# Kernel optimization log

Measured on AMD Instinct MI355X. Metric: run time of the kernel, lower is better.

## Reference

```python
import jax, jax.numpy as jnp
import numpy as np

B, T, C, H = 8, 2048, 256, 4
D = C // H  # head_dim = 64
SCALE = D ** -0.5


def setup_inputs() -> dict:
    key = jax.random.key(0)
    ks = jax.random.split(key, 5)
    return {
        "x": jax.random.normal(ks[0], (B, T, C), dtype=jnp.float32),
        "Wqkv": jax.random.normal(ks[1], (C, 3 * C), dtype=jnp.float32) * (C ** -0.5),
        "bqkv": jax.random.normal(ks[2], (3 * C,), dtype=jnp.float32) * 0.02,
        "Wproj": jax.random.normal(ks[3], (C, C), dtype=jnp.float32) * (C ** -0.5),
        "bproj": jax.random.normal(ks[4], (C,), dtype=jnp.float32) * 0.02,
    }


def reference(x, Wqkv, bqkv, Wproj, bproj):
    b, t, c = x.shape
    # QKV projection -> (3, B, H, T, D) matching torch permute(2,0,3,1,4)
    qkv = (x @ Wqkv + bqkv).reshape(b, t, 3, H, D)
    qkv = jnp.transpose(qkv, (2, 0, 3, 1, 4))
    q, k, v = qkv[0], qkv[1], qkv[2]  # each (B, H, T, D)
    # Full T x T scores (faithful to the original non-fused implementation)
    attn = jnp.einsum("bhqd,bhkd->bhqk", q, k) * SCALE
    causal = jnp.triu(jnp.ones((t, t), dtype=bool), k=1)  # True above diagonal
    attn = jnp.where(causal, -jnp.inf, attn)
    attn = jax.nn.softmax(attn, axis=-1)
    # dropout is identity in eval mode
    out = jnp.einsum("bhqk,bhkd->bhqd", attn, v)  # (B, H, T, D)
    out = jnp.transpose(out, (0, 2, 1, 3)).reshape(b, t, c)
    return out @ Wproj + bproj
```

## Files before the change

kernel.cpp:

```cpp
#include <hip/hip_runtime.h>
#include <hip/hip_bf16.h>
#include <math.h>

#define BATCH 8
#define SEQ   2048
#define CH    256
#define NH    4
#define HD    64
#define NQB   (SEQ / 64)
#define QSCALE 0.18033688011112042f

typedef short  bfrag __attribute__((ext_vector_type(8)));
typedef float  ffrag __attribute__((ext_vector_type(4)));
typedef unsigned short ushort_t;

__device__ __forceinline__ unsigned short f2bf(float f) {
    union { float f; unsigned int u; } v; v.f = f;
    unsigned int r = v.u + 0x7FFF + ((v.u >> 16) & 1);
    return (unsigned short)(r >> 16);
}
__device__ __forceinline__ unsigned int pack2(float a, float b) {
    const __hip_bfloat162 p = __float22bfloat162_rn(make_float2(a, b));
    return *(const unsigned int*)&p;
}

#define WQN (CH * 3 * CH)
#define WPN (CH * CH)
#define XN  (BATCH * SEQ * CH)
#define XN8 (XN / 8)

__global__ __launch_bounds__(256) void prep_kernel(
    const float* __restrict__ x,
    const float* __restrict__ Wqkv, const float* __restrict__ Wproj,
    ushort_t* __restrict__ xb,
    ushort_t* __restrict__ WqkvT, ushort_t* __restrict__ WprojT) {
    const int fid = blockIdx.x * 256 + threadIdx.x;
    if (fid < XN8) {
        const float4 a = *(const float4*)&x[(size_t)fid * 8];
        const float4 c = *(const float4*)&x[(size_t)fid * 8 + 4];
        uint4 pk;
        pk.x = pack2(a.x, a.y); pk.y = pack2(a.z, a.w);
        pk.z = pack2(c.x, c.y); pk.w = pack2(c.z, c.w);
        *(uint4*)&xb[(size_t)fid * 8] = pk;
    } else {
        const int id = fid - XN8;
        if (id < WQN) {
            const int n = id >> 8, k = id & 255;
            WqkvT[n * CH + k] = f2bf(Wqkv[k * (3 * CH) + n]);
        } else if (id < WQN + WPN) {
            const int i = id - WQN;
            const int n = i >> 8, k = i & 255;
            WprojT[n * CH + k] = f2bf(Wproj[k * CH + n]);
        }
    }
}

#define GLS 72

__global__ __launch_bounds__(256) void qkv_mfma_kernel(
    const ushort_t* __restrict__ xb, const ushort_t* __restrict__ Wt,
    const float* __restrict__ bias,
    ushort_t* __restrict__ Qb, ushort_t* __restrict__ Kb,
    ushort_t* __restrict__ Vtb) {
    __shared__ ushort_t smem[2 * 128 * GLS];
    ushort_t* As = smem;
    ushort_t* Bs = smem + 128 * GLS;

    const int tid = threadIdx.x;
    const int wv  = tid >> 6;
    const int ln  = tid & 63;
    const int l15 = ln & 15;
    const int l4  = ln >> 4;
    const int wr  = wv >> 1;
    const int wc  = wv & 1;
    const int n0  = blockIdx.x * 128;
    const int m0  = blockIdx.y * 128;

    ffrag acc[4][4];
    #pragma unroll
    for (int i = 0; i < 4; i++)
        #pragma unroll
        for (int j = 0; j < 4; j++) acc[i][j] = (ffrag){0.f, 0.f, 0.f, 0.f};

    for (int k0 = 0; k0 < CH; k0 += 64) {
        #pragma unroll
        for (int r = 0; r < 4; r++) {
            const int fid = tid + r * 256;
            const int row = fid >> 3, c8 = (fid & 7) * 8;
            *(uint4*)&As[row * GLS + c8] = *(const uint4*)&xb[(size_t)(m0 + row) * CH + k0 + c8];
            *(uint4*)&Bs[row * GLS + c8] = *(const uint4*)&Wt[(n0 + row) * CH + k0 + c8];
        }
        __syncthreads();
        #pragma unroll
        for (int kk = 0; kk < 64; kk += 32) {
            bfrag a[4], b[4];
            #pragma unroll
            for (int i = 0; i < 4; i++)
                a[i] = *(const bfrag*)&As[(wr * 64 + i * 16 + l15) * GLS + kk + l4 * 8];
            #pragma unroll
            for (int j = 0; j < 4; j++)
                b[j] = *(const bfrag*)&Bs[(wc * 64 + j * 16 + l15) * GLS + kk + l4 * 8];
            #pragma unroll
            for (int i = 0; i < 4; i++)
                #pragma unroll
                for (int j = 0; j < 4; j++)
                    acc[i][j] = __builtin_amdgcn_mfma_f32_16x16x32_bf16(a[i], b[j], acc[i][j], 0, 0, 0);
        }
        __syncthreads();
    }

    const int mat = n0 >> 8;
    const int b   = m0 >> 11;
    const int t0  = m0 & (SEQ - 1);
    ushort_t (*T)[136] = (ushort_t(*)[136])smem;

    if (mat < 2) {
        const float sc = (mat == 0) ? QSCALE : 1.0f;
        #pragma unroll
        for (int j = 0; j < 4; j++) {
            const int n_local = wc * 64 + j * 16 + l15;
            const float bj = bias[n0 + n_local];
            #pragma unroll
            for (int i = 0; i < 4; i++) {
                const int m_base = wr * 64 + i * 16 + l4 * 4;
                #pragma unroll
                for (int r = 0; r < 4; r++)
                    T[m_base + r][n_local] = f2bf((acc[i][j][r] + bj) * sc);
            }
        }
        __syncthreads();
        ushort_t* dst = (mat == 0) ? Qb : Kb;
        #pragma unroll
        for (int rr = 0; rr < 8; rr++) {
            const int fid = tid + rr * 256;
            const int row = fid >> 4;
            const int c8  = (fid & 15) * 8;
            const int n_glob = n0 + c8;
            const int h = (n_glob >> 6) & 3;
            const int d = n_glob & 63;
            *(uint4*)&dst[((size_t)((b * NH + h) * SEQ) + t0 + row) * HD + d] =
                *(const uint4*)&T[row][c8];
        }
    } else {
        #pragma unroll
        for (int j = 0; j < 4; j++) {
            const int n_local = wc * 64 + j * 16 + l15;
            const float bj = bias[n0 + n_local];
            #pragma unroll
            for (int i = 0; i < 4; i++) {
                const int m_base = wr * 64 + i * 16 + l4 * 4;
                ushort4 pk;
                pk.x = f2bf(acc[i][j][0] + bj);
                pk.y = f2bf(acc[i][j][1] + bj);
                pk.z = f2bf(acc[i][j][2] + bj);
                pk.w = f2bf(acc[i][j][3] + bj);
                *(ushort4*)&T[n_local][m_base] = pk;
            }
        }
        __syncthreads();
        #pragma unroll
        for (int rr = 0; rr < 8; rr++) {
            const int fid = tid + rr * 256;
            const int row = fid >> 4;
            const int c8  = (fid & 15) * 8;
            const int n_glob = n0 + row;
            const int h = (n_glob >> 6) & 3;
            const int d = n_glob & 63;
            *(uint4*)&Vtb[(size_t)((b * NH + h) * HD + d) * SEQ + t0 + c8] =
                *(const uint4*)&T[row][c8];
        }
    }
}

__global__ __launch_bounds__(256, 4) void attn_mfma_kernel(
    const ushort_t* __restrict__ Qb, const ushort_t* __restrict__ Kb,
    const ushort_t* __restrict__ Vtb, ushort_t* __restrict__ out) {
    __shared__ ushort_t Ps[64 * 64];
    __shared__ ushort_t KV[4 * 64 * 64];

    const int tid = threadIdx.x;
    const int wv  = tid >> 6;
    const int ln  = tid & 63;
    const int l15 = ln & 15;
    const int l4  = ln >> 4;
    const int e   = l15 & 7;

    const int L  = blockIdx.x;
    const int g  = L & 255;
    const int s4 = L >> 8;
    const int v  = g >> 5;
    const int qb = (s4 == 0) ? (31 - v) : (s4 == 1) ? (16 + v) : (s4 == 2) ? (15 - v) : v;
    const int bh = g & 31;
    const int b  = bh >> 2;
    const int h  = bh & 3;

    const ushort_t* Qp = Qb + ((size_t)(bh * SEQ + qb * 64 + wv * 16 + l15)) * HD + l4 * 8;
    const bfrag bq0 = *(const bfrag*)Qp;
    const bfrag bq1 = *(const bfrag*)(Qp + 32);

    const ushort_t* Kbase = Kb  + (size_t)bh * SEQ * HD;
    const ushort_t* Vbase = Vtb + (size_t)bh * HD * SEQ;
    const int srow  = tid >> 3;
    const int sc    = tid & 7;
    const int goffA = srow * 64 + sc * 8;
    const int voffA = srow * SEQ + sc * 8;
    const int soffA = srow * 64 + ((sc ^ (srow & 7)) * 8);

    const int kf0 = l15 * 64 + ((l4 ^ e) * 8);
    const int pf0 = (wv * 16 + l15) * 64 + ((l4 ^ e) * 8);
    const int pp  = e >> 1;
    const int pwb = (wv * 16 + l15) * 64 + (((l4 >> 1) ^ (e & 1)) * 8) + (l4 & 1) * 4;

    uint4 kK0, kK1, kV0, kV1;
    kK0 = *(const uint4*)&Kbase[goffA];
    kK1 = *(const uint4*)&Kbase[goffA + 32 * 64];
    kV0 = *(const uint4*)&Vbase[voffA];
    kV1 = *(const uint4*)&Vbase[voffA + 32 * SEQ];
    *(uint4*)&KV[soffA]          = kK0;
    *(uint4*)&KV[soffA + 2048]   = kK1;
    *(uint4*)&KV[8192 + soffA]        = kV0;
    *(uint4*)&KV[8192 + soffA + 2048] = kV1;
    if (qb >= 1) {
        kK0 = *(const uint4*)&Kbase[4096 + goffA];
        kK1 = *(const uint4*)&Kbase[4096 + goffA + 32 * 64];
        kV0 = *(const uint4*)&Vbase[64 + voffA];
        kV1 = *(const uint4*)&Vbase[64 + voffA + 32 * SEQ];
    }

    ffrag o[4];
    #pragma unroll
    for (int n = 0; n < 4; n++) o[n] = (ffrag){0.f, 0.f, 0.f, 0.f};
    float l_q = 0.f;
    const int qg_l = qb * 64 + wv * 16 + l15;

    for (int kt = 0; kt <= qb; kt++) {
        if (kt > 0) {
            const int kb = (kt & 1) * 4096;
            *(uint4*)&KV[kb + soffA]          = kK0;
            *(uint4*)&KV[kb + soffA + 2048]   = kK1;
            *(uint4*)&KV[8192 + kb + soffA]        = kV0;
            *(uint4*)&KV[8192 + kb + soffA + 2048] = kV1;
            if (kt < qb) {
                const ushort_t* Kp  = Kbase + (kt + 1) * 4096;
                const ushort_t* Vtp = Vbase + (kt + 1) * 64;
                kK0 = *(const uint4*)&Kp[goffA];
                kK1 = *(const uint4*)&Kp[goffA + 32 * 64];
                kV0 = *(const uint4*)&Vtp[voffA];
                kV1 = *(const uint4*)&Vtp[voffA + 32 * SEQ];
            }
        }
        __syncthreads();

        const ushort_t* Kbuf = KV + (kt & 1) * 4096;
        const ushort_t* Vbuf = KV + 8192 + (kt & 1) * 4096;

        ffrag s[4];
        #pragma unroll
        for (int n = 0; n < 4; n++) {
            const bfrag ak0 = *(const bfrag*)&Kbuf[n * 1024 + kf0];
            const bfrag ak1 = *(const bfrag*)&Kbuf[n * 1024 + (kf0 ^ 32)];
            ffrag z = (ffrag){0.f, 0.f, 0.f, 0.f};
            z = __builtin_amdgcn_mfma_f32_16x16x32_bf16(ak0, bq0, z, 0, 0, 0);
            z = __builtin_amdgcn_mfma_f32_16x16x32_bf16(ak1, bq1, z, 0, 0, 0);
            s[n] = z;
        }
        if (kt == qb) {
            #pragma unroll
            for (int n = 0; n < 4; n++)
                #pragma unroll
                for (int r = 0; r < 4; r++)
                    if (kt * 64 + n * 16 + l4 * 4 + r > qg_l) s[n][r] = -INFINITY;
        }

        float rs = 0.f;
        #pragma unroll
        for (int n = 0; n < 4; n++)
            #pragma unroll
            for (int r = 0; r < 4; r++) {
                const float p = __builtin_amdgcn_exp2f(s[n][r]);
                s[n][r] = p;
                rs += p;
            }
        rs += __shfl_xor(rs, 16);
        rs += __shfl_xor(rs, 32);
        l_q += rs;

        #pragma unroll
        for (int n = 0; n < 4; n++) {
            uint2 pk;
            pk.x = pack2(s[n][0], s[n][1]);
            pk.y = pack2(s[n][2], s[n][3]);
            *(uint2*)&Ps[pwb + ((n ^ pp) << 4)] = pk;
        }

        const bfrag ap0 = *(const bfrag*)&Ps[pf0];
        const bfrag ap1 = *(const bfrag*)&Ps[pf0 ^ 32];
        #pragma unroll
        for (int n = 0; n < 4; n++) {
            const bfrag av0 = *(const bfrag*)&Vbuf[n * 1024 + kf0];
            const bfrag av1 = *(const bfrag*)&Vbuf[n * 1024 + (kf0 ^ 32)];
            o[n] = __builtin_amdgcn_mfma_f32_16x16x32_bf16(av0, ap0, o[n], 0, 0, 0);
            o[n] = __builtin_amdgcn_mfma_f32_16x16x32_bf16(av1, ap1, o[n], 0, 0, 0);
        }
    }

    const float li = 1.0f / l_q;
    const int tq = qb * 64 + wv * 16 + l15;
    ushort_t* op = out + (size_t)(b * SEQ + tq) * CH + h * HD;
    #pragma unroll
    for (int n = 0; n < 4; n++) {
        ushort4 pk;
        pk.x = f2bf(o[n][0] * li);
        pk.y = f2bf(o[n][1] * li);
        pk.z = f2bf(o[n][2] * li);
        pk.w = f2bf(o[n][3] * li);
        *(ushort4*)&op[n * 16 + l4 * 4] = pk;
    }
}

__global__ __launch_bounds__(256) void proj_mfma_kernel(
    const ushort_t* __restrict__ Ab, const ushort_t* __restrict__ Wt,
    const float* __restrict__ bias, float* __restrict__ O) {
    __shared__ ushort_t smem[(128 + 64) * GLS];
    ushort_t* As = smem;
    ushort_t* Bs = smem + 128 * GLS;

    const int tid = threadIdx.x;
    const int wv  = tid >> 6;
    const int ln  = tid & 63;
    const int l15 = ln & 15;
    const int l4  = ln >> 4;
    const int wr  = wv >> 1;
    const int wc  = wv & 1;
    const int n0  = blockIdx.x * 64;
    const int m0  = blockIdx.y * 128;

    ffrag acc[4][2];
    #pragma unroll
    for (int i = 0; i < 4; i++)
        #pragma unroll
        for (int j = 0; j < 2; j++) acc[i][j] = (ffrag){0.f, 0.f, 0.f, 0.f};

    for (int k0 = 0; k0 < CH; k0 += 64) {
        #pragma unroll
        for (int r = 0; r < 4; r++) {
            const int fid = tid + r * 256;
            const int row = fid >> 3, c8 = (fid & 7) * 8;
            *(uint4*)&As[row * GLS + c8] = *(const uint4*)&Ab[(size_t)(m0 + row) * CH + k0 + c8];
        }
        #pragma unroll
        for (int r = 0; r < 2; r++) {
            const int fid = tid + r * 256;
            const int row = fid >> 3, c8 = (fid & 7) * 8;
            *(uint4*)&Bs[row * GLS + c8] = *(const uint4*)&Wt[(n0 + row) * CH + k0 + c8];
        }
        __syncthreads();
        #pragma unroll
        for (int kk = 0; kk < 64; kk += 32) {
            bfrag a[4], b[2];
            #pragma unroll
            for (int i = 0; i < 4; i++)
                a[i] = *(const bfrag*)&As[(wr * 64 + i * 16 + l15) * GLS + kk + l4 * 8];
            #pragma unroll
            for (int j = 0; j < 2; j++)
                b[j] = *(const bfrag*)&Bs[(wc * 32 + j * 16 + l15) * GLS + kk + l4 * 8];
            #pragma unroll
            for (int i = 0; i < 4; i++)
                #pragma unroll
                for (int j = 0; j < 2; j++)
                    acc[i][j] = __builtin_amdgcn_mfma_f32_16x16x32_bf16(a[i], b[j], acc[i][j], 0, 0, 0);
        }
        __syncthreads();
    }

    #pragma unroll
    for (int j = 0; j < 2; j++) {
        const int n = n0 + wc * 32 + j * 16 + l15;
        const float bj = bias[n];
        #pragma unroll
        for (int i = 0; i < 4; i++) {
            const int m = m0 + wr * 64 + i * 16 + l4 * 4;
            #pragma unroll
            for (int r = 0; r < 4; r++)
                O[(size_t)(m + r) * CH + n] = acc[i][j][r] + bj;
        }
    }
}

extern "C" void kernel_launch(void* const* d_in, const int* in_sizes, int n_in,
                              void* d_out, int out_size, void* d_ws, size_t ws_size,
                              hipStream_t stream) {
    const float* x     = (const float*)d_in[0];
    const float* Wqkv  = (const float*)d_in[1];
    const float* bqkv  = (const float*)d_in[2];
    const float* Wproj = (const float*)d_in[3];
    const float* bproj = (const float*)d_in[4];
    float* out = (float*)d_out;

    const size_t BHTD = (size_t)BATCH * NH * SEQ * HD;
    ushort_t* WqkvT  = (ushort_t*)d_ws;
    ushort_t* WprojT = WqkvT + (size_t)3 * CH * CH;
    ushort_t* Qb     = WprojT + (size_t)CH * CH;
    ushort_t* Kb     = Qb + BHTD;
    ushort_t* Vtb    = Kb + BHTD;
    ushort_t* attn_b = Vtb + BHTD;
    ushort_t* xb     = attn_b;

    const int M = BATCH * SEQ;

    {
        const int total = XN8 + WQN + WPN;
        prep_kernel<<<(total + 255) / 256, 256, 0, stream>>>(x, Wqkv, Wproj, xb, WqkvT, WprojT);
    }
    {
        dim3 grid((3 * CH) / 128, M / 128);
        qkv_mfma_kernel<<<grid, 256, 0, stream>>>(xb, WqkvT, bqkv, Qb, Kb, Vtb);
    }
    {
        attn_mfma_kernel<<<dim3(NQB * BATCH * NH), 256, 0, stream>>>(Qb, Kb, Vtb, attn_b);
    }
    {
        dim3 grid(CH / 64, M / 128);
        proj_mfma_kernel<<<grid, 256, 0, stream>>>(attn_b, WprojT, bproj, out);
    }
}
```

Baseline: 135.7 us.

## Process 128 query rows per attention block to double K/V tile reuse

Each attention block now covers a 128-row query tile, with each wavefront handling two 16-row subtiles, so every K/V tile staged in shared memory feeds twice as many MFMAs. This halves the global and LDS traffic for K/V per query row and halves the grid to 512 blocks, with a reworked causal pairing of tiles to balance load. The cost is more registers per thread (occupancy hint lowered to 2), a larger P buffer, and fewer blocks to spread over the CUs. Causal masking now covers the last two key tiles of the diagonal.

```diff
diff --git a/kernel.cpp b/kernel.cpp
--- a/kernel.cpp
+++ b/kernel.cpp
@@ -7,7 +7,6 @@
 #define CH    256
 #define NH    4
 #define HD    64
-#define NQB   (SEQ / 64)
 #define QSCALE 0.18033688011112042f
 
 typedef short  bfrag __attribute__((ext_vector_type(8)));
@@ -172,10 +171,10 @@
     }
 }
 
-__global__ __launch_bounds__(256, 4) void attn_mfma_kernel(
+__global__ __launch_bounds__(256, 2) void attn_mfma_kernel(
     const ushort_t* __restrict__ Qb, const ushort_t* __restrict__ Kb,
     const ushort_t* __restrict__ Vtb, ushort_t* __restrict__ out) {
-    __shared__ ushort_t Ps[64 * 64];
+    __shared__ ushort_t Ps[128 * 64];
     __shared__ ushort_t KV[4 * 64 * 64];
 
     const int tid = threadIdx.x;
@@ -187,16 +186,20 @@
 
     const int L  = blockIdx.x;
     const int g  = L & 255;
-    const int s4 = L >> 8;
+    const int s2 = L >> 8;
     const int v  = g >> 5;
-    const int qb = (s4 == 0) ? (31 - v) : (s4 == 1) ? (16 + v) : (s4 == 2) ? (15 - v) : v;
+    const int qt = (s2 == 0) ? (15 - v) : v;
     const int bh = g & 31;
     const int b  = bh >> 2;
     const int h  = bh & 3;
-
-    const ushort_t* Qp = Qb + ((size_t)(bh * SEQ + qb * 64 + wv * 16 + l15)) * HD + l4 * 8;
-    const bfrag bq0 = *(const bfrag*)Qp;
-    const bfrag bq1 = *(const bfrag*)(Qp + 32);
+    const int nkt  = 2 * qt + 2;
+    const int qrow = qt * 128 + wv * 32;
+
+    const ushort_t* Qp0 = Qb + ((size_t)(bh * SEQ + qrow + l15)) * HD + l4 * 8;
+    const bfrag bq00 = *(const bfrag*)Qp0;
+    const bfrag bq01 = *(const bfrag*)(Qp0 + 32);
+    const bfrag bq10 = *(const bfrag*)(Qp0 + 16 * HD);
+    const bfrag bq11 = *(const bfrag*)(Qp0 + 16 * HD + 32);
 
     const ushort_t* Kbase = Kb  + (size_t)bh * SEQ * HD;
     const ushort_t* Vbase = Vtb + (size_t)bh * HD * SEQ;
@@ -206,10 +209,12 @@
     const int voffA = srow * SEQ + sc * 8;
     const int soffA = srow * 64 + ((sc ^ (srow & 7)) * 8);
 
-    const int kf0 = l15 * 64 + ((l4 ^ e) * 8);
-    const int pf0 = (wv * 16 + l15) * 64 + ((l4 ^ e) * 8);
-    const int pp  = e >> 1;
-    const int pwb = (wv * 16 + l15) * 64 + (((l4 >> 1) ^ (e & 1)) * 8) + (l4 & 1) * 4;
+    const int kf0  = l15 * 64 + ((l4 ^ e) * 8);
+    const int pf00 = (wv * 32 + l15) * 64 + ((l4 ^ e) * 8);
+    const int pf10 = pf00 + 16 * 64;
+    const int pp   = e >> 1;
+    const int pwb0 = (wv * 32 + l15) * 64 + (((l4 >> 1) ^ (e & 1)) * 8) + (l4 & 1) * 4;
+    const int pwb1 = pwb0 + 16 * 64;
 
     uint4 kK0, kK1, kV0, kV1;
     kK0 = *(const uint4*)&Kbase[goffA];
@@ -220,27 +225,29 @@
     *(uint4*)&KV[soffA + 2048]   = kK1;
     *(uint4*)&KV[8192 + soffA]        = kV0;
     *(uint4*)&KV[8192 + soffA + 2048] = kV1;
-    if (qb >= 1) {
-        kK0 = *(const uint4*)&Kbase[4096 + goffA];
-        kK1 = *(const uint4*)&Kbase[4096 + goffA + 32 * 64];
-        kV0 = *(const uint4*)&Vbase[64 + voffA];
-        kV1 = *(const uint4*)&Vbase[64 + voffA + 32 * SEQ];
-    }
-
-    ffrag o[4];
+    kK0 = *(const uint4*)&Kbase[4096 + goffA];
+    kK1 = *(const uint4*)&Kbase[4096 + goffA + 32 * 64];
+    kV0 = *(const uint4*)&Vbase[64 + voffA];
+    kV1 = *(const uint4*)&Vbase[64 + voffA + 32 * SEQ];
+
+    ffrag o0[4], o1[4];
     #pragma unroll
-    for (int n = 0; n < 4; n++) o[n] = (ffrag){0.f, 0.f, 0.f, 0.f};
-    float l_q = 0.f;
-    const int qg_l = qb * 64 + wv * 16 + l15;
-
-    for (int kt = 0; kt <= qb; kt++) {
+    for (int n = 0; n < 4; n++) {
+        o0[n] = (ffrag){0.f, 0.f, 0.f, 0.f};
+        o1[n] = (ffrag){0.f, 0.f, 0.f, 0.f};
+    }
+    float l0 = 0.f, l1 = 0.f;
+    const int qg0 = qrow + l15;
+    const int qg1 = qg0 + 16;
+
+    for (int kt = 0; kt < nkt; kt++) {
         if (kt > 0) {
             const int kb = (kt & 1) * 4096;
             *(uint4*)&KV[kb + soffA]          = kK0;
             *(uint4*)&KV[kb + soffA + 2048]   = kK1;
             *(uint4*)&KV[8192 + kb + soffA]        = kV0;
             *(uint4*)&KV[8192 + kb + soffA + 2048] = kV1;
-            if (kt < qb) {
+            if (kt < nkt - 1) {
                 const ushort_t* Kp  = Kbase + (kt + 1) * 4096;
                 const ushort_t* Vtp = Vbase + (kt + 1) * 64;
                 kK0 = *(const uint4*)&Kp[goffA];
@@ -254,67 +261,94 @@
         const ushort_t* Kbuf = KV + (kt & 1) * 4096;
         const ushort_t* Vbuf = KV + 8192 + (kt & 1) * 4096;
 
-        ffrag s[4];
+        ffrag s0[4], s1[4];
         #pragma unroll
         for (int n = 0; n < 4; n++) {
             const bfrag ak0 = *(const bfrag*)&Kbuf[n * 1024 + kf0];
             const bfrag ak1 = *(const bfrag*)&Kbuf[n * 1024 + (kf0 ^ 32)];
-            ffrag z = (ffrag){0.f, 0.f, 0.f, 0.f};
-            z = __builtin_amdgcn_mfma_f32_16x16x32_bf16(ak0, bq0, z, 0, 0, 0);
-            z = __builtin_amdgcn_mfma_f32_16x16x32_bf16(ak1, bq1, z, 0, 0, 0);
-            s[n] = z;
-        }
-        if (kt == qb) {
+            ffrag z0 = (ffrag){0.f, 0.f, 0.f, 0.f};
+            z0 = __builtin_amdgcn_mfma_f32_16x16x32_bf16(ak0, bq00, z0, 0, 0, 0);
+            z0 = __builtin_amdgcn_mfma_f32_16x16x32_bf16(ak1, bq01, z0, 0, 0, 0);
+            s0[n] = z0;
+            ffrag z1 = (ffrag){0.f, 0.f, 0.f, 0.f};
+            z1 = __builtin_amdgcn_mfma_f32_16x16x32_bf16(ak0, bq10, z1, 0, 0, 0);
+            z1 = __builtin_amdgcn_mfma_f32_16x16x32_bf16(ak1, bq11, z1, 0, 0, 0);
+            s1[n] = z1;
+        }
+        if (kt >= nkt - 2) {
             #pragma unroll
             for (int n = 0; n < 4; n++)
                 #pragma unroll
-                for (int r = 0; r < 4; r++)
-                    if (kt * 64 + n * 16 + l4 * 4 + r > qg_l) s[n][r] = -INFINITY;
-        }
-
-        float rs = 0.f;
+                for (int r = 0; r < 4; r++) {
+                    const int kk_ = kt * 64 + n * 16 + l4 * 4 + r;
+                    if (kk_ > qg0) s0[n][r] = -INFINITY;
+                    if (kk_ > qg1) s1[n][r] = -INFINITY;
+                }
+        }
+
+        float rs0 = 0.f, rs1 = 0.f;
         #pragma unroll
         for (int n = 0; n < 4; n++)
             #pragma unroll
             for (int r = 0; r < 4; r++) {
-                const float p = __builtin_amdgcn_exp2f(s[n][r]);
-                s[n][r] = p;
-                rs += p;
+                const float p0 = __builtin_amdgcn_exp2f(s0[n][r]);
+                s0[n][r] = p0;
+                rs0 += p0;
+                const float p1 = __builtin_amdgcn_exp2f(s1[n][r]);
+                s1[n][r] = p1;
+                rs1 += p1;
             }
-        rs += __shfl_xor(rs, 16);
-        rs += __shfl_xor(rs, 32);
-        l_q += rs;
+        rs0 += __shfl_xor(rs0, 16);
+        rs0 += __shfl_xor(rs0, 32);
+        l0 += rs0;
+        rs1 += __shfl_xor(rs1, 16);
+        rs1 += __shfl_xor(rs1, 32);
+        l1 += rs1;
 
         #pragma unroll
         for (int n = 0; n < 4; n++) {
-            uint2 pk;
-            pk.x = pack2(s[n][0], s[n][1]);
-            pk.y = pack2(s[n][2], s[n][3]);
-            *(uint2*)&Ps[pwb + ((n ^ pp) << 4)] = pk;
-        }
-
-        const bfrag ap0 = *(const bfrag*)&Ps[pf0];
-        const bfrag ap1 = *(const bfrag*)&Ps[pf0 ^ 32];
+            uint2 pk0, pk1;
+            pk0.x = pack2(s0[n][0], s0[n][1]);
+            pk0.y = pack2(s0[n][2], s0[n][3]);
+            *(uint2*)&Ps[pwb0 + ((n ^ pp) << 4)] = pk0;
+            pk1.x = pack2(s1[n][0], s1[n][1]);
+            pk1.y = pack2(s1[n][2], s1[n][3]);
+            *(uint2*)&Ps[pwb1 + ((n ^ pp) << 4)] = pk1;
+        }
+
+        const bfrag ap00 = *(const bfrag*)&Ps[pf00];
+        const bfrag ap01 = *(const bfrag*)&Ps[pf00 ^ 32];
+        const bfrag ap10 = *(const bfrag*)&Ps[pf10];
+        const bfrag ap11 = *(const bfrag*)&Ps[pf10 ^ 32];
         #pragma unroll
         for (int n = 0; n < 4; n++) {
             const bfrag av0 = *(const bfrag*)&Vbuf[n * 1024 + kf0];
             const bfrag av1 = *(const bfrag*)&Vbuf[n * 1024 + (kf0 ^ 32)];
-            o[n] = __builtin_amdgcn_mfma_f32_16x16x32_bf16(av0, ap0, o[n], 0, 0, 0);
-            o[n] = __builtin_amdgcn_mfma_f32_16x16x32_bf16(av1, ap1, o[n], 0, 0, 0);
-        }
-    }
-
-    const float li = 1.0f / l_q;
-    const int tq = qb * 64 + wv * 16 + l15;
-    ushort_t* op = out + (size_t)(b * SEQ + tq) * CH + h * HD;
+            o0[n] = __builtin_amdgcn_mfma_f32_16x16x32_bf16(av0, ap00, o0[n], 0, 0, 0);
+            o0[n] = __builtin_amdgcn_mfma_f32_16x16x32_bf16(av1, ap01, o0[n], 0, 0, 0);
+            o1[n] = __builtin_amdgcn_mfma_f32_16x16x32_bf16(av0, ap10, o1[n], 0, 0, 0);
+            o1[n] = __builtin_amdgcn_mfma_f32_16x16x32_bf16(av1, ap11, o1[n], 0, 0, 0);
+        }
+    }
+
+    const float li0 = 1.0f / l0;
+    const float li1 = 1.0f / l1;
+    const int tq0 = qrow + l15;
+    ushort_t* op0 = out + (size_t)(b * SEQ + tq0) * CH + h * HD;
+    ushort_t* op1 = op0 + 16 * CH;
     #pragma unroll
     for (int n = 0; n < 4; n++) {
-        ushort4 pk;
-        pk.x = f2bf(o[n][0] * li);
-        pk.y = f2bf(o[n][1] * li);
-        pk.z = f2bf(o[n][2] * li);
-        pk.w = f2bf(o[n][3] * li);
-        *(ushort4*)&op[n * 16 + l4 * 4] = pk;
+        ushort4 pk0, pk1;
+        pk0.x = f2bf(o0[n][0] * li0);
+        pk0.y = f2bf(o0[n][1] * li0);
+        pk0.z = f2bf(o0[n][2] * li0);
+        pk0.w = f2bf(o0[n][3] * li0);
+        *(ushort4*)&op0[n * 16 + l4 * 4] = pk0;
+        pk1.x = f2bf(o1[n][0] * li1);
+        pk1.y = f2bf(o1[n][1] * li1);
+        pk1.z = f2bf(o1[n][2] * li1);
+        pk1.w = f2bf(o1[n][3] * li1);
+        *(ushort4*)&op1[n * 16 + l4 * 4] = pk1;
     }
 }
 
@@ -417,7 +451,7 @@
         qkv_mfma_kernel<<<grid, 256, 0, stream>>>(xb, WqkvT, bqkv, Qb, Kb, Vtb);
     }
     {
-        attn_mfma_kernel<<<dim3(NQB * BATCH * NH), 256, 0, stream>>>(Qb, Kb, Vtb, attn_b);
+        attn_mfma_kernel<<<dim3(512), 256, 0, stream>>>(Qb, Kb, Vtb, attn_b);
     }
     {
         dim3 grid(CH / 64, M / 128);
```

Result: slower. 140.9 us (+3.8%).

## Use direct global-to-LDS loads with XOR swizzle in QKV GEMM, defer row-sum reduction

Applied to the files above, without the earlier changes.

The QKV projection GEMM now loads tiles with global_load_lds (bypassing registers) into an unpadded LDS layout using an XOR swizzle, and reads fragments with the matching swizzle to avoid bank conflicts. In the attention kernel, the per-tile cross-lane shuffle reduction of the softmax row sum is moved out of the loop into a single reduction at the end, and s_setprio raises wave priority around the MFMA blocks. The aim is to cut VGPR traffic and LDS conflicts in the GEMM and per-iteration shuffle overhead in attention. The swizzle must match exactly between the store and read sides or results become wrong.

```diff
diff --git a/kernel.cpp b/kernel.cpp
--- a/kernel.cpp
+++ b/kernel.cpp
@@ -13,6 +13,7 @@
 typedef short  bfrag __attribute__((ext_vector_type(8)));
 typedef float  ffrag __attribute__((ext_vector_type(4)));
 typedef unsigned short ushort_t;
+typedef unsigned int u32;
 
 __device__ __forceinline__ unsigned short f2bf(float f) {
     union { float f; unsigned int u; } v; v.f = f;
@@ -22,6 +23,11 @@
 __device__ __forceinline__ unsigned int pack2(float a, float b) {
     const __hip_bfloat162 p = __float22bfloat162_rn(make_float2(a, b));
     return *(const unsigned int*)&p;
+}
+__device__ __forceinline__ void gload16(const ushort_t* g, ushort_t* l) {
+    __builtin_amdgcn_global_load_lds(
+        (const __attribute__((address_space(1))) u32*)g,
+        (__attribute__((address_space(3))) u32*)l, 16, 0, 0);
 }
 
 #define WQN (CH * 3 * CH)
@@ -62,20 +68,24 @@
     const float* __restrict__ bias,
     ushort_t* __restrict__ Qb, ushort_t* __restrict__ Kb,
     ushort_t* __restrict__ Vtb) {
-    __shared__ ushort_t smem[2 * 128 * GLS];
+    __shared__ ushort_t smem[128 * 136];
     ushort_t* As = smem;
-    ushort_t* Bs = smem + 128 * GLS;
+    ushort_t* Bs = smem + 128 * 64;
 
     const int tid = threadIdx.x;
     const int wv  = tid >> 6;
     const int ln  = tid & 63;
     const int l15 = ln & 15;
     const int l4  = ln >> 4;
+    const int e   = l15 & 7;
     const int wr  = wv >> 1;
     const int wc  = wv & 1;
     const int n0  = blockIdx.x * 128;
     const int m0  = blockIdx.y * 128;
 
+    const int grow = ln >> 3;
+    const int swz  = ((ln & 7) ^ grow) * 8;
+
     ffrag acc[4][4];
     #pragma unroll
     for (int i = 0; i < 4; i++)
@@ -84,22 +94,25 @@
 
     for (int k0 = 0; k0 < CH; k0 += 64) {
         #pragma unroll
-        for (int r = 0; r < 4; r++) {
-            const int fid = tid + r * 256;
-            const int row = fid >> 3, c8 = (fid & 7) * 8;
-            *(uint4*)&As[row * GLS + c8] = *(const uint4*)&xb[(size_t)(m0 + row) * CH + k0 + c8];
-            *(uint4*)&Bs[row * GLS + c8] = *(const uint4*)&Wt[(n0 + row) * CH + k0 + c8];
+        for (int i = 0; i < 4; i++) {
+            const int rowA = (i * 4 + wv) * 8 + grow;
+            gload16(&xb[(size_t)(m0 + rowA) * CH + k0 + swz], &As[(i * 4 + wv) * 512]);
+            gload16(&Wt[(size_t)(n0 + rowA) * CH + k0 + swz], &Bs[(i * 4 + wv) * 512]);
         }
         __syncthreads();
         #pragma unroll
         for (int kk = 0; kk < 64; kk += 32) {
             bfrag a[4], b[4];
             #pragma unroll
-            for (int i = 0; i < 4; i++)
-                a[i] = *(const bfrag*)&As[(wr * 64 + i * 16 + l15) * GLS + kk + l4 * 8];
-            #pragma unroll
-            for (int j = 0; j < 4; j++)
-                b[j] = *(const bfrag*)&Bs[(wc * 64 + j * 16 + l15) * GLS + kk + l4 * 8];
+            for (int i = 0; i < 4; i++) {
+                const int R = wr * 64 + i * 16 + l15;
+                a[i] = *(const bfrag*)&As[R * 64 + ((((kk >> 3) + l4) ^ e) * 8)];
+            }
+            #pragma unroll
+            for (int j = 0; j < 4; j++) {
+                const int R = wc * 64 + j * 16 + l15;
+                b[j] = *(const bfrag*)&Bs[R * 64 + ((((kk >> 3) + l4) ^ e) * 8)];
+            }
             #pragma unroll
             for (int i = 0; i < 4; i++)
                 #pragma unroll
@@ -255,6 +268,7 @@
         const ushort_t* Vbuf = KV + 8192 + (kt & 1) * 4096;
 
         ffrag s[4];
+        __builtin_amdgcn_s_setprio(1);
         #pragma unroll
         for (int n = 0; n < 4; n++) {
             const bfrag ak0 = *(const bfrag*)&Kbuf[n * 1024 + kf0];
@@ -264,6 +278,7 @@
             z = __builtin_amdgcn_mfma_f32_16x16x32_bf16(ak1, bq1, z, 0, 0, 0);
             s[n] = z;
         }
+        __builtin_amdgcn_s_setprio(0);
         if (kt == qb) {
             #pragma unroll
             for (int n = 0; n < 4; n++)
@@ -272,18 +287,14 @@
                     if (kt * 64 + n * 16 + l4 * 4 + r > qg_l) s[n][r] = -INFINITY;
         }
 
-        float rs = 0.f;
         #pragma unroll
         for (int n = 0; n < 4; n++)
             #pragma unroll
             for (int r = 0; r < 4; r++) {
                 const float p = __builtin_amdgcn_exp2f(s[n][r]);
                 s[n][r] = p;
-                rs += p;
-            }
-        rs += __shfl_xor(rs, 16);
-        rs += __shfl_xor(rs, 32);
-        l_q += rs;
+                l_q += p;
+            }
 
         #pragma unroll
         for (int n = 0; n < 4; n++) {
@@ -295,6 +306,7 @@
 
         const bfrag ap0 = *(const bfrag*)&Ps[pf0];
         const bfrag ap1 = *(const bfrag*)&Ps[pf0 ^ 32];
+        __builtin_amdgcn_s_setprio(1);
         #pragma unroll
         for (int n = 0; n < 4; n++) {
             const bfrag av0 = *(const bfrag*)&Vbuf[n * 1024 + kf0];
@@ -302,7 +314,11 @@
             o[n] = __builtin_amdgcn_mfma_f32_16x16x32_bf16(av0, ap0, o[n], 0, 0, 0);
             o[n] = __builtin_amdgcn_mfma_f32_16x16x32_bf16(av1, ap1, o[n], 0, 0, 0);
         }
-    }
+        __builtin_amdgcn_s_setprio(0);
+    }
+
+    l_q += __shfl_xor(l_q, 16);
+    l_q += __shfl_xor(l_q, 32);
 
     const float li = 1.0f / l_q;
     const int tq = qb * 64 + wv * 16 + l15;
```

Measured after the change: 133.5 us. Within noise of the previous version (-1.6%).
